# Optimization experiments

Measured on AMD Instinct MI355X. Metric: run time of the kernel, lower is better.

The kernel has to match this reference:

```python
import jax, jax.numpy as jnp
import numpy as np

IN_DIM = 3
GRID_LEVEL = 7
FEAT_DIMS = 2
HIDDEN = 128
BOUND = 1.0
W0_SINE = 56.0  # n_levels**feature_dims - n_levels = 8**2 - 8
N = 131072


def setup_inputs() -> dict:
    key = jax.random.key(0)
    ks = jax.random.split(key, 10)
    return {
        "in_pos": jax.random.uniform(ks[0], (N, IN_DIM), jnp.float32, -1.0, 1.0),
        "grid_feats": jax.random.uniform(ks[1], (N, IN_DIM + GRID_LEVEL * FEAT_DIMS), jnp.float32),
        "ffn_A": jax.random.normal(ks[2], (GRID_LEVEL, FEAT_DIMS, HIDDEN), jnp.float32) * 5.0,
        "ffn_sigma": jnp.ones((GRID_LEVEL,), jnp.float32),
        "W0": jax.random.uniform(ks[3], (HIDDEN, IN_DIM), jnp.float32, -1.0 / IN_DIM, 1.0 / IN_DIM),
        "b0": jax.random.uniform(ks[4], (HIDDEN,), jnp.float32, -1.0 / IN_DIM, 1.0 / IN_DIM),
        "W_mid": jax.random.uniform(ks[5], (GRID_LEVEL, HIDDEN, HIDDEN), jnp.float32) * (2.0 * np.sqrt(6.0 / HIDDEN) / W0_SINE) - np.sqrt(6.0 / HIDDEN) / W0_SINE,
        "b_mid": jnp.zeros((GRID_LEVEL, HIDDEN), jnp.float32),
        "W_high": jax.random.uniform(ks[6], (GRID_LEVEL, HIDDEN, HIDDEN), jnp.float32) * (2.0 * np.sqrt(6.0 / HIDDEN) / W0_SINE) - np.sqrt(6.0 / HIDDEN) / W0_SINE,
        "b_high": jnp.zeros((GRID_LEVEL, HIDDEN), jnp.float32),
    }


def reference(in_pos, grid_feats, ffn_A, ffn_sigma, W0, b0, W_mid, b_mid, W_high, b_high):
    x = in_pos / BOUND                     # [N, 3], in [-1, 1]
    pos01 = (in_pos + BOUND) / (2.0 * BOUND)  # [N, 3], in [0, 1]

    # grid branch: slice off the first in_dim columns, reshape to [L, N, F]
    gx = grid_feats[..., IN_DIM:].reshape(-1, GRID_LEVEL, FEAT_DIMS).transpose(1, 0, 2)
    A = ffn_A * ffn_sigma[:, None, None]   # [L, F, H]
    grid_x = jnp.sin(jnp.einsum('lnf,lfh->lnh', gx, (2.0 * jnp.pi) * A))  # [L, N, H]

    # first SIREN layer
    x = jnp.sin(W0_SINE * (x @ W0.T + b0))  # [N, H]

    def step(carry, layer):
        x, buf = carry
        Wm, bm, Wh, bh, g = layer
        x = jnp.sin(W0_SINE * (x @ Wm.T + bm))
        x = g + x                                  # residual add of grid features
        buf = buf + jnp.sin(W0_SINE * (x @ Wh.T + bh))  # high-freq accumulation
        return (x, buf), None

    buf0 = jnp.zeros((x.shape[0], HIDDEN), x.dtype)
    (_, buf), _ = jax.lax.scan(step, (x, buf0), (W_mid, b_mid, W_high, b_high, grid_x))

    return jnp.concatenate([pos01, buf / GRID_LEVEL], axis=-1)  # [N, 3 + 128]
```

## Files before the change

kernel.cpp:

```cpp
#include <hip/hip_runtime.h>
#include <hip/hip_bf16.h>


typedef __bf16 bf16_t;
typedef __attribute__((ext_vector_type(8))) __bf16 bf16x8;
typedef __attribute__((ext_vector_type(4))) float f32x4;
typedef __attribute__((ext_vector_type(16))) float f32x16;

#define C56R 8.9126768f
#define INV7 0.14285714285714285f

#define OFF_WMF   0
#define OFF_WMFLO 229376
#define OFF_WHF   458752
#define OFF_EPM   688128

union ChunkU { bf16x8 v; unsigned int d[4]; };

__device__ __forceinline__ unsigned short bfbits(float x) {
  bf16_t b = (bf16_t)x;
  return __builtin_bit_cast(unsigned short, b);
}
__device__ __forceinline__ float bf2f(unsigned short u) {
  return __builtin_bit_cast(float, (unsigned int)u << 16);
}
__device__ __forceinline__ void pack2(float v0, float v1,
                                      unsigned int& ph, unsigned int& pl) {
  unsigned short h0 = bfbits(v0), h1 = bfbits(v1);
  ph = (unsigned int)h0 | ((unsigned int)h1 << 16);
  float l0 = v0 - bf2f(h0), l1 = v1 - bf2f(h1);
  pl = (unsigned int)bfbits(l0) | ((unsigned int)bfbits(l1) << 16);
}

__global__ void ffb_prep(const float* __restrict__ ffnA, const float* __restrict__ sigma,
                         const float* __restrict__ Wm, const float* __restrict__ bm,
                         const float* __restrict__ Wh, const float* __restrict__ bh,
                         unsigned char* __restrict__ ws) {
  int i = blockIdx.x * 256 + threadIdx.x;
  bf16_t* wmf = (bf16_t*)(ws + OFF_WMF);
  bf16_t* wml = (bf16_t*)(ws + OFF_WMFLO);
  bf16_t* whf = (bf16_t*)(ws + OFF_WHF);
  {
    int j    = i & 7;
    int lane = (i >> 3) & 63;
    int kc   = (i >> 9) & 7;
    int mt   = (i >> 12) & 3;
    int it   = i >> 14;
    int ho   = (mt << 5) + (lane & 31);
    int hin  = (kc << 4) + ((lane >> 5) << 3) + j;
    int src  = (it << 14) + (ho << 7) + hin;
    float w  = Wm[src];
    bf16_t h = (bf16_t)w;
    wmf[i] = h;
    wml[i] = (bf16_t)(w - (float)h);
    whf[i] = (bf16_t)Wh[src];
  }
  if (i < 896) {
    int r  = i & 15;
    int mt = (i >> 4) & 3;
    int hf = (i >> 6) & 1;
    int it = i >> 7;
    int h  = (mt << 5) + (r & 3) + ((r >> 2) << 3) + (hf << 2);
    float sg = sigma[it];
    f32x4 e;
    e.x = ffnA[it * 256 + h] * sg;
    e.y = ffnA[it * 256 + 128 + h] * sg;
    e.z = C56R * bm[it * 128 + h];
    e.w = C56R * bh[it * 128 + h];
    ((f32x4*)(ws + OFF_EPM))[i] = e;
  }
}

__launch_bounds__(256, 6)
__global__ void ffb_main(const float* __restrict__ pos,
                         const float* __restrict__ gfeat,
                         const float* __restrict__ W0,
                         const float* __restrict__ b0,
                         const unsigned char* __restrict__ ws,
                         float* __restrict__ out) {
  __shared__ __align__(16) unsigned char sX[16384];

  const int tid  = threadIdx.x;
  const int L    = tid & 63;
  const int sub  = tid >> 6;
  const int p    = L & 31;
  const int hf   = L >> 5;
  const int n    = (blockIdx.x << 5) + p;

  const bf16_t* __restrict__ WMH = (const bf16_t*)(ws + OFF_WMF);
  const bf16_t* __restrict__ WML = (const bf16_t*)(ws + OFF_WMFLO);
  const bf16_t* __restrict__ WHF = (const bf16_t*)(ws + OFF_WHF);
  const f32x4*  __restrict__ EPM = (const f32x4*)(ws + OFF_EPM);
  const float*  __restrict__ EPW = (const float*)(ws + OFF_EPM);

  const float p0 = pos[n * 3 + 0], p1 = pos[n * 3 + 1], p2 = pos[n * 3 + 2];
  if (sub == 0 && hf == 0) {
    out[(size_t)n * 131 + 0] = (p0 + 1.f) * 0.5f;
    out[(size_t)n * 131 + 1] = (p1 + 1.f) * 0.5f;
    out[(size_t)n * 131 + 2] = (p2 + 1.f) * 0.5f;
  }

  #pragma unroll
  for (int cc = 0; cc < 2; ++cc) {
    const int c = (sub << 1) + cc;
    ChunkU chi, clo;
    #pragma unroll
    for (int jp = 0; jp < 4; ++jp) {
      int h0 = (c << 4) + (hf << 3) + 2 * jp;
      float d0 = __builtin_fmaf(p2, W0[h0*3+2], __builtin_fmaf(p1, W0[h0*3+1], p0 * W0[h0*3+0]));
      float d1 = __builtin_fmaf(p2, W0[h0*3+5], __builtin_fmaf(p1, W0[h0*3+4], p0 * W0[h0*3+3]));
      float v0 = __builtin_amdgcn_sinf(C56R * (d0 + b0[h0]));
      float v1 = __builtin_amdgcn_sinf(C56R * (d1 + b0[h0 + 1]));
      pack2(v0, v1, chi.d[jp], clo.d[jp]);
    }
    *(bf16x8*)(sX + (c << 10) + (L << 4))        = chi.v;
    *(bf16x8*)(sX + 8192 + (c << 10) + (L << 4)) = clo.v;
  }
  __syncthreads();

  f32x16 buf;
  #pragma unroll
  for (int r = 0; r < 16; ++r) buf[r] = 0.f;

  for (int it = 0; it < 8; ++it) {
    if (it > 0) {
      f32x16 acc;
      #pragma unroll
      for (int r = 0; r < 16; ++r) acc[r] = 0.f;
      const bf16_t* wb = WHF + ((it - 1) << 14) + (sub << 12) + (L << 3);
      bf16x8 fnext = *(const bf16x8*)(wb);
      #pragma unroll
      for (int kc = 0; kc < 8; ++kc) {
        bf16x8 f = fnext;
        if (kc < 7) fnext = *(const bf16x8*)(wb + ((kc + 1) << 9));
        bf16x8 xhc = *(const bf16x8*)(sX + (kc << 10) + (L << 4));
        acc = __builtin_amdgcn_mfma_f32_32x32x16_bf16(f, xhc, acc, 0, 0, 0);
      }
      const int eb = ((((it - 1) << 1) + hf) << 2) + sub;
      #pragma unroll
      for (int r = 0; r < 16; ++r) {
        float cbh = EPW[(eb * 16 + r) * 4 + 3];
        buf[r] += __builtin_amdgcn_sinf(__builtin_fmaf(acc[r], C56R, cbh));
      }
    }

    if (it < 7) {
      f32x16 acc;
      #pragma unroll
      for (int r = 0; r < 16; ++r) acc[r] = 0.f;
      const bf16_t* wh = WMH + (it << 14) + (sub << 12) + (L << 3);
      const bf16_t* wl = WML + (it << 14) + (sub << 12) + (L << 3);
      bf16x8 fhnext = *(const bf16x8*)(wh);
      bf16x8 flnext = *(const bf16x8*)(wl);
      #pragma unroll
      for (int kc = 0; kc < 8; ++kc) {
        bf16x8 fh = fhnext;
        bf16x8 fl = flnext;
        if (kc < 7) {
          fhnext = *(const bf16x8*)(wh + ((kc + 1) << 9));
          flnext = *(const bf16x8*)(wl + ((kc + 1) << 9));
        }
        bf16x8 xhc = *(const bf16x8*)(sX + (kc << 10) + (L << 4));
        bf16x8 xlc = *(const bf16x8*)(sX + 8192 + (kc << 10) + (L << 4));
        acc = __builtin_amdgcn_mfma_f32_32x32x16_bf16(fh, xhc, acc, 0, 0, 0);
        acc = __builtin_amdgcn_mfma_f32_32x32x16_bf16(fl, xhc, acc, 0, 0, 0);
        acc = __builtin_amdgcn_mfma_f32_32x32x16_bf16(fh, xlc, acc, 0, 0, 0);
      }

      __syncthreads();

      const float g0 = gfeat[n * 17 + 3 + 2 * it];
      const float g1 = gfeat[n * 17 + 4 + 2 * it];
      const int eb = (((it << 1) + hf) << 2) + sub;
      #pragma unroll
      for (int rp = 0; rp < 8; ++rp) {
        const int r = 2 * rp;
        f32x4 e0 = EPM[eb * 16 + r];
        f32x4 e1 = EPM[eb * 16 + r + 1];
        float sg0 = __builtin_amdgcn_sinf(__builtin_amdgcn_fractf(__builtin_fmaf(g1, e0.y, g0 * e0.x)));
        float sg1 = __builtin_amdgcn_sinf(__builtin_amdgcn_fractf(__builtin_fmaf(g1, e1.y, g0 * e1.x)));
        float sm0 = __builtin_amdgcn_sinf(__builtin_fmaf(acc[r],     C56R, e0.z));
        float sm1 = __builtin_amdgcn_sinf(__builtin_fmaf(acc[r + 1], C56R, e1.z));
        unsigned int phv, plv;
        pack2(sg0 + sm0, sg1 + sm1, phv, plv);
        const int h   = (sub << 5) + (r & 3) + ((r >> 2) << 3) + (hf << 2);
        const int off = ((h >> 4) << 10) + ((p + (((h >> 3) & 1) << 5)) << 4) + ((h & 7) << 1);
        *(unsigned int*)(sX + off)        = phv;
        *(unsigned int*)(sX + 8192 + off) = plv;
      }
      __syncthreads();
    }
  }

  float* op = out + (size_t)n * 131 + 3;
  #pragma unroll
  for (int r = 0; r < 16; ++r) {
    const int h = (sub << 5) + (r & 3) + ((r >> 2) << 3) + (hf << 2);
    op[h] = buf[r] * INV7;
  }
}

extern "C" void kernel_launch(void* const* d_in, const int* in_sizes, int n_in,
                              void* d_out, int out_size, void* d_ws, size_t ws_size,
                              hipStream_t stream) {
  (void)in_sizes; (void)n_in; (void)out_size; (void)ws_size;
  const float* pos   = (const float*)d_in[0];
  const float* gfeat = (const float*)d_in[1];
  const float* ffnA  = (const float*)d_in[2];
  const float* sigma = (const float*)d_in[3];
  const float* W0    = (const float*)d_in[4];
  const float* b0    = (const float*)d_in[5];
  const float* Wm    = (const float*)d_in[6];
  const float* bm    = (const float*)d_in[7];
  const float* Wh    = (const float*)d_in[8];
  const float* bh    = (const float*)d_in[9];
  float* out = (float*)d_out;
  unsigned char* ws = (unsigned char*)d_ws;

  hipLaunchKernelGGL(ffb_prep, dim3(448), dim3(256), 0, stream,
                     ffnA, sigma, Wm, bm, Wh, bh, ws);
  hipLaunchKernelGGL(ffb_main, dim3(4096), dim3(256), 0, stream,
                     pos, gfeat, W0, b0, ws, out);
}
```

Measured before the change: 282.5 us.

## Register-prefetch next layer weights and stage epilogue params in LDS

Weight fragments for the mid and high layers are now loaded a full stage ahead into register arrays (24 bf16x8 per thread), so the global latency overlaps with the preceding MFMA and sine work instead of being prefetched one k-chunk at a time. The per-layer epilogue constants are copied once into shared memory rather than read from global each layer. Launch bounds drop from 6 to 3 blocks per CU to make room for the extra registers, and shared memory per block roughly doubles, reducing occupancy and latency hiding across waves.

```diff
diff --git a/kernel.cpp b/kernel.cpp
--- a/kernel.cpp
+++ b/kernel.cpp
@@ -71,14 +71,17 @@
   }
 }
 
-__launch_bounds__(256, 6)
+__launch_bounds__(256, 3)
 __global__ void ffb_main(const float* __restrict__ pos,
                          const float* __restrict__ gfeat,
                          const float* __restrict__ W0,
                          const float* __restrict__ b0,
                          const unsigned char* __restrict__ ws,
                          float* __restrict__ out) {
-  __shared__ __align__(16) unsigned char sX[16384];
+  __shared__ __align__(16) unsigned char smem[30720];
+  unsigned char* sX = smem;
+  f32x4* sEPv = (f32x4*)(smem + 16384);
+  float* sEPf = (float*)(smem + 16384);
 
   const int tid  = threadIdx.x;
   const int L    = tid & 63;
@@ -91,7 +94,23 @@
   const bf16_t* __restrict__ WML = (const bf16_t*)(ws + OFF_WMFLO);
   const bf16_t* __restrict__ WHF = (const bf16_t*)(ws + OFF_WHF);
   const f32x4*  __restrict__ EPM = (const f32x4*)(ws + OFF_EPM);
-  const float*  __restrict__ EPW = (const float*)(ws + OFF_EPM);
+
+  bf16x8 mh[8], ml[8], hfr[8];
+  {
+    const bf16_t* wh0 = WMH + (sub << 12) + (L << 3);
+    const bf16_t* wl0 = WML + (sub << 12) + (L << 3);
+    #pragma unroll
+    for (int kc = 0; kc < 8; ++kc) {
+      mh[kc] = *(const bf16x8*)(wh0 + (kc << 9));
+      ml[kc] = *(const bf16x8*)(wl0 + (kc << 9));
+    }
+  }
+
+  #pragma unroll
+  for (int c = 0; c < 4; ++c) {
+    int idx = tid + (c << 8);
+    if (idx < 896) sEPv[idx] = EPM[idx];
+  }
 
   const float p0 = pos[n * 3 + 0], p1 = pos[n * 3 + 1], p2 = pos[n * 3 + 2];
   if (sub == 0 && hf == 0) {
@@ -122,49 +141,53 @@
   #pragma unroll
   for (int r = 0; r < 16; ++r) buf[r] = 0.f;
 
+  #pragma unroll 1
   for (int it = 0; it < 8; ++it) {
     if (it > 0) {
       f32x16 acc;
       #pragma unroll
       for (int r = 0; r < 16; ++r) acc[r] = 0.f;
-      const bf16_t* wb = WHF + ((it - 1) << 14) + (sub << 12) + (L << 3);
-      bf16x8 fnext = *(const bf16x8*)(wb);
       #pragma unroll
       for (int kc = 0; kc < 8; ++kc) {
-        bf16x8 f = fnext;
-        if (kc < 7) fnext = *(const bf16x8*)(wb + ((kc + 1) << 9));
         bf16x8 xhc = *(const bf16x8*)(sX + (kc << 10) + (L << 4));
-        acc = __builtin_amdgcn_mfma_f32_32x32x16_bf16(f, xhc, acc, 0, 0, 0);
+        acc = __builtin_amdgcn_mfma_f32_32x32x16_bf16(hfr[kc], xhc, acc, 0, 0, 0);
       }
       const int eb = ((((it - 1) << 1) + hf) << 2) + sub;
       #pragma unroll
       for (int r = 0; r < 16; ++r) {
-        float cbh = EPW[(eb * 16 + r) * 4 + 3];
+        float cbh = sEPf[(eb * 16 + r) * 4 + 3];
         buf[r] += __builtin_amdgcn_sinf(__builtin_fmaf(acc[r], C56R, cbh));
       }
     }
 
     if (it < 7) {
+      {
+        const bf16_t* wb = WHF + (it << 14) + (sub << 12) + (L << 3);
+        #pragma unroll
+        for (int kc = 0; kc < 8; ++kc)
+          hfr[kc] = *(const bf16x8*)(wb + (kc << 9));
+      }
+
       f32x16 acc;
       #pragma unroll
       for (int r = 0; r < 16; ++r) acc[r] = 0.f;
-      const bf16_t* wh = WMH + (it << 14) + (sub << 12) + (L << 3);
-      const bf16_t* wl = WML + (it << 14) + (sub << 12) + (L << 3);
-      bf16x8 fhnext = *(const bf16x8*)(wh);
-      bf16x8 flnext = *(const bf16x8*)(wl);
       #pragma unroll
       for (int kc = 0; kc < 8; ++kc) {
-        bf16x8 fh = fhnext;
-        bf16x8 fl = flnext;
-        if (kc < 7) {
-          fhnext = *(const bf16x8*)(wh + ((kc + 1) << 9));
-          flnext = *(const bf16x8*)(wl + ((kc + 1) << 9));
-        }
         bf16x8 xhc = *(const bf16x8*)(sX + (kc << 10) + (L << 4));
         bf16x8 xlc = *(const bf16x8*)(sX + 8192 + (kc << 10) + (L << 4));
-        acc = __builtin_amdgcn_mfma_f32_32x32x16_bf16(fh, xhc, acc, 0, 0, 0);
-        acc = __builtin_amdgcn_mfma_f32_32x32x16_bf16(fl, xhc, acc, 0, 0, 0);
-        acc = __builtin_amdgcn_mfma_f32_32x32x16_bf16(fh, xlc, acc, 0, 0, 0);
+        acc = __builtin_amdgcn_mfma_f32_32x32x16_bf16(mh[kc], xhc, acc, 0, 0, 0);
+        acc = __builtin_amdgcn_mfma_f32_32x32x16_bf16(ml[kc], xhc, acc, 0, 0, 0);
+        acc = __builtin_amdgcn_mfma_f32_32x32x16_bf16(mh[kc], xlc, acc, 0, 0, 0);
+      }
+
+      if (it < 6) {
+        const bf16_t* wh = WMH + ((it + 1) << 14) + (sub << 12) + (L << 3);
+        const bf16_t* wl = WML + ((it + 1) << 14) + (sub << 12) + (L << 3);
+        #pragma unroll
+        for (int kc = 0; kc < 8; ++kc) {
+          mh[kc] = *(const bf16x8*)(wh + (kc << 9));
+          ml[kc] = *(const bf16x8*)(wl + (kc << 9));
+        }
       }
 
       __syncthreads();
@@ -175,8 +198,8 @@
       #pragma unroll
       for (int rp = 0; rp < 8; ++rp) {
         const int r = 2 * rp;
-        f32x4 e0 = EPM[eb * 16 + r];
-        f32x4 e1 = EPM[eb * 16 + r + 1];
+        f32x4 e0 = sEPv[eb * 16 + r];
+        f32x4 e1 = sEPv[eb * 16 + r + 1];
         float sg0 = __builtin_amdgcn_sinf(__builtin_amdgcn_fractf(__builtin_fmaf(g1, e0.y, g0 * e0.x)));
         float sg1 = __builtin_amdgcn_sinf(__builtin_amdgcn_fractf(__builtin_fmaf(g1, e1.y, g0 * e1.x)));
         float sm0 = __builtin_amdgcn_sinf(__builtin_fmaf(acc[r],     C56R, e0.z));
```

New measurement: 266.2 us. 1.06x faster.
